# Optimization experiments

Hardware: AMD Instinct MI355X
Metric: run time of the kernel (lower is better)

## Reference

```python
import jax, jax.numpy as jnp
import numpy as np
from jax import lax

B, T, I, H, C = 64, 512, 512, 1024, 1000


def _lstm_layer(x, W_ih, W_hh, b_ih, b_hh):
    # x: [B, T, in]; W_ih: [4H, in]; W_hh: [4H, H]; biases: [4H]
    # Precompute input projections for all timesteps (one big GEMM).
    xW = jnp.einsum('bti,gi->btg', x, W_ih) + b_ih + b_hh  # [B, T, 4H]
    h0 = jnp.zeros((x.shape[0], W_hh.shape[1]), x.dtype)
    c0 = jnp.zeros_like(h0)

    def step(carry, xw_t):
        h, c = carry
        gates = xw_t + h @ W_hh.T  # [B, 4H]
        i, f, g, o = jnp.split(gates, 4, axis=-1)  # PyTorch gate order i,f,g,o
        i = jax.nn.sigmoid(i)
        f = jax.nn.sigmoid(f)
        g = jnp.tanh(g)
        o = jax.nn.sigmoid(o)
        c = f * c + i * g
        h = o * jnp.tanh(c)
        return (h, c), h

    (h_T, c_T), hs = lax.scan(step, (h0, c0), jnp.swapaxes(xW, 0, 1))
    return jnp.swapaxes(hs, 0, 1), h_T  # [B, T, H], [B, H]


def setup_inputs() -> dict:
    key = jax.random.key(0)
    ks = jax.random.split(key, 11)
    s_i = 1.0 / np.sqrt(H)
    u = lambda k, shape: jax.random.uniform(k, shape, jnp.float32, -s_i, s_i)
    return {
        'x': jax.random.normal(ks[0], (B, T, I), jnp.float32),
        'W_ih0': u(ks[1], (4 * H, I)),
        'W_hh0': u(ks[2], (4 * H, H)),
        'b_ih0': u(ks[3], (4 * H,)),
        'b_hh0': u(ks[4], (4 * H,)),
        'W_ih1': u(ks[5], (4 * H, H)),
        'W_hh1': u(ks[6], (4 * H, H)),
        'b_ih1': u(ks[7], (4 * H,)),
        'b_hh1': u(ks[8], (4 * H,)),
        'W_d': u(ks[9], (C, H)),
        'b_d': u(ks[10], (C,)),
    }


def reference(x, W_ih0, W_hh0, b_ih0, b_hh0, W_ih1, W_hh1, b_ih1, b_hh1, W_d, b_d):
    h1_seq, _ = _lstm_layer(x, W_ih0, W_hh0, b_ih0, b_hh0)
    _, h_last = _lstm_layer(h1_seq, W_ih1, W_hh1, b_ih1, b_hh1)
    return h_last @ W_d.T + b_d  # [B, num_classes]
```

## Files before the change

### kernel.cpp

```cpp
#include <hip/hip_runtime.h>

typedef short short8 __attribute__((ext_vector_type(8)));
typedef float f32x4 __attribute__((ext_vector_type(4)));
typedef float f32x16 __attribute__((ext_vector_type(16)));
typedef int i32x4 __attribute__((ext_vector_type(4)));
typedef unsigned short u16;

#define NBLK 256
#define BDIM 512
#define BB 64
#define TT 512
#define II 512
#define HH 1024
#define NCLS 1000
#define HBUF (BB*HH)

__device__ __forceinline__ u16 f2bf(float f) {
  union { float f; unsigned u; } v; v.f = f;
  unsigned u = v.u;
  u += 0x7fffu + ((u >> 16) & 1u);
  return (u16)(u >> 16);
}

__device__ __forceinline__ short8 cvt8(f32x4 a, f32x4 b) {
  short8 v;
  v[0] = (short)f2bf(a[0]); v[1] = (short)f2bf(a[1]);
  v[2] = (short)f2bf(a[2]); v[3] = (short)f2bf(a[3]);
  v[4] = (short)f2bf(b[0]); v[5] = (short)f2bf(b[1]);
  v[6] = (short)f2bf(b[2]); v[7] = (short)f2bf(b[3]);
  return v;
}

__device__ __forceinline__ unsigned ld_rlx(const unsigned* p) {
  return __hip_atomic_load(p, __ATOMIC_RELAXED, __HIP_MEMORY_SCOPE_AGENT);
}
__device__ __forceinline__ void st_rlx(unsigned* p, unsigned v) {
  __hip_atomic_store(p, v, __ATOMIC_RELAXED, __HIP_MEMORY_SCOPE_AGENT);
}
__device__ __forceinline__ void wave_wait_ge(const unsigned* p, unsigned tgt) {
  while (ld_rlx(p) < tgt) __builtin_amdgcn_s_sleep(1);
}

__global__ void cvt_x(const float* __restrict__ x, u16* __restrict__ xb, int n8) {
  int i = blockIdx.x * blockDim.x + threadIdx.x;
  const int stride = gridDim.x * blockDim.x;
  for (; i < n8; i += stride) {
    f32x4 a = ((const f32x4*)x)[2 * i];
    f32x4 b = ((const f32x4*)x)[2 * i + 1];
    ((short8*)xb)[i] = cvt8(a, b);
  }
}

#define ISSUE8(arr, OFF)                                                     \
  _Pragma("unroll") for (int i_ = 0; i_ < 8; ++i_)                           \
    asm volatile("global_load_dwordx4 %0, %1, off sc0 sc1"                   \
                 : "=v"(arr[i_]) : "v"(lanep + ((OFF) + i_) * 16));
#define MFMA8(arr, OFF)                                                      \
  _Pragma("unroll") for (int i_ = 0; i_ < 8; ++i_) {                         \
    union { i32x4 q; short8 s; } u_; u_.q = arr[i_];                         \
    acc = __builtin_amdgcn_mfma_f32_32x32x16_bf16(u_.s, breg[B0 + (OFF) + i_],\
                                                  acc, 0, 0, 0); }
#define VMWAIT0 asm volatile("s_waitcnt vmcnt(0)" ::: "memory")
#define VMWAIT8 asm volatile("s_waitcnt vmcnt(8)" ::: "memory")
#define SCHEDB  __builtin_amdgcn_sched_barrier(0)

template<int N, int B0, int MH>
__device__ __forceinline__ void run_coh(const u16* lanep,
                                        const short8 (&breg)[MH], f32x16& acc) {
  static_assert(N == 8 || N == 16 || N == 24 || N == 32, "");
  i32x4 avA[8], avB[8];
  if constexpr (N == 8) {
    ISSUE8(avA, 0);
    VMWAIT0; SCHEDB; MFMA8(avA, 0);
  } else if constexpr (N == 16) {
    ISSUE8(avA, 0); ISSUE8(avB, 8);
    VMWAIT8; SCHEDB; MFMA8(avA, 0);
    VMWAIT0; SCHEDB; MFMA8(avB, 8);
  } else if constexpr (N == 24) {
    ISSUE8(avA, 0); ISSUE8(avB, 8);
    VMWAIT8; SCHEDB; MFMA8(avA, 0); ISSUE8(avA, 16);
    VMWAIT8; SCHEDB; MFMA8(avB, 8);
    VMWAIT0; SCHEDB; MFMA8(avA, 16);
  } else {
    ISSUE8(avA, 0); ISSUE8(avB, 8);
    VMWAIT8; SCHEDB; MFMA8(avA, 0); ISSUE8(avA, 16);
    VMWAIT8; SCHEDB; MFMA8(avB, 8); ISSUE8(avB, 24);
    VMWAIT8; SCHEDB; MFMA8(avA, 16);
    VMWAIT0; SCHEDB; MFMA8(avB, 24);
  }
}

template<int N, int B0, int MH>
__device__ __forceinline__ void run_pb(const u16* lanep,
                                       const short8 (&breg)[MH], f32x16& acc) {
#pragma unroll
  for (int i = 0; i < N; ++i) {
    short8 av = *(const short8*)(lanep + i * 16);
    acc = __builtin_amdgcn_mfma_f32_32x32x16_bf16(av, breg[B0 + i], acc, 0, 0, 0);
  }
}

template<int N, int B0, int MH>
__device__ __forceinline__ void run_pf(const float* lanep,
                                       const short8 (&breg)[MH], f32x16& acc) {
#pragma unroll
  for (int i = 0; i < N; ++i) {
    short8 av = cvt8(*(const f32x4*)(lanep + i * 16),
                     *(const f32x4*)(lanep + i * 16 + 4));
    acc = __builtin_amdgcn_mfma_f32_32x32x16_bf16(av, breg[B0 + i], acc, 0, 0, 0);
  }
}

template<bool XBF>
__global__ __launch_bounds__(BDIM, 2) void lstm2_fused(
    const float* __restrict__ x, const u16* __restrict__ xb,
    const float* __restrict__ Wih0, const float* __restrict__ Whh0,
    const float* __restrict__ bih0, const float* __restrict__ bhh0,
    const float* __restrict__ Wih1, const float* __restrict__ Whh1,
    const float* __restrict__ bih1, const float* __restrict__ bhh1,
    u16* __restrict__ ring,
    u16* __restrict__ h1buf,
    float* __restrict__ h1f,
    unsigned* __restrict__ bar)
{
  __shared__ float g4[4][32][68];
  __shared__ float blds[64];

  const bool isL1 = (blockIdx.x >= 128);
  const int wgl = isL1 ? (int)blockIdx.x - 128 : (int)blockIdx.x;
  const int ug = wgl >> 1, bg = wgl & 1;
  const int j0 = ug * 16;
  const int rowoff = bg * 32;

  const int lane = threadIdx.x & 63;
  const int wid = threadIdx.x >> 6;
  const int gr = wid & 1, kq = wid >> 1;
  const int sub8 = (lane >> 5) << 3;
  const int rl = gr * 32 + (lane & 31);
  const int rglob = ((rl >> 4) << 10) + j0 + (rl & 15);
  const int arow = rowoff + (lane & 31);

  if (threadIdx.x < 64) {
    int u = threadIdx.x;
    int r = ((u >> 4) << 10) + j0 + (u & 15);
    blds[u] = isL1 ? (bih1[r] + bhh1[r]) : (bih0[r] + bhh0[r]);
  }
  __syncthreads();

  const int tb = threadIdx.x >> 4;
  const int tu = threadIdx.x & 15;

  unsigned* const arrA = bar;
  unsigned* const relA = bar + 64;
  unsigned* const arrB = bar + 128;
  unsigned* const relB = bar + 192;

  float c_state = 0.f;

  auto step_tail = [&](const f32x16& acc, u16* hout, unsigned ringtgt, bool wf,
                       unsigned* arr, unsigned* rel, int t) {
    const int col = lane & 31;
    const int rbase = (lane >> 5) << 2;
#pragma unroll
    for (int r = 0; r < 16; ++r) {
      int brow = rbase + (r & 3) + ((r >> 2) << 3);
      g4[kq][brow][gr * 32 + col] = acc[r];
    }
    __syncthreads();
    float gv[4];
#pragma unroll
    for (int g = 0; g < 4; ++g)
      gv[g] = g4[0][tb][g * 16 + tu] + g4[1][tb][g * 16 + tu]
            + g4[2][tb][g * 16 + tu] + g4[3][tb][g * 16 + tu]
            + blds[g * 16 + tu];
    float gi = 1.f / (1.f + __expf(-gv[0]));
    float gf = 1.f / (1.f + __expf(-gv[1]));
    float e2 = __expf(2.f * fminf(15.f, fmaxf(-15.f, gv[2])));
    float gg = (e2 - 1.f) / (e2 + 1.f);
    float go = 1.f / (1.f + __expf(-gv[3]));
    c_state = gf * c_state + gi * gg;
    float e2c = __expf(2.f * fminf(15.f, fmaxf(-15.f, c_state)));
    float th = (e2c - 1.f) / (e2c + 1.f);
    float hval = go * th;
    if (ringtgt) wave_wait_ge(relB, ringtgt);
    unsigned hu = (unsigned)f2bf(hval);
    unsigned nbv = (unsigned)__shfl_xor((int)hu, 1);
    if ((tu & 1) == 0) {
      unsigned packed = hu | (nbv << 16);
      unsigned* dst = (unsigned*)(hout + (size_t)(rowoff + tb) * HH + j0 + tu);
      st_rlx(dst, packed);
    }
    if (wf) h1f[(size_t)(rowoff + tb) * HH + j0 + tu] = hval;
    __syncthreads();
    if (threadIdx.x == 0) {
      unsigned old = atomicAdd(arr, 1u);
      if (old == (unsigned)(128 * (t + 1) - 1)) st_rlx(rel, (unsigned)(t + 1));
    }
  };

  if (!isL1) {
    short8 breg[24];
#pragma unroll
    for (int i = 0; i < 24; ++i) {
      int k = kq * 384 + i * 16 + sub8;
      const float* src = (k < II) ? (Wih0 + (size_t)rglob * II + k)
                                  : (Whh0 + (size_t)rglob * HH + (k - II));
      breg[i] = cvt8(*(const f32x4*)src, *(const f32x4*)(src + 4));
    }

    for (int t = 0; t < TT; ++t) {
      f32x16 acc = {};
      const u16* hb = ring + (size_t)((t + 2) % 3) * HBUF + (size_t)arow * HH;
      if (XBF) {
        const u16* xl = xb + (size_t)arow * ((size_t)TT * II) + (size_t)t * II
                        + kq * 384 + sub8;
        if (kq == 0)      run_pb<24, 0>(xl, breg, acc);
        else if (kq == 1) { run_pb<8, 0>(xl, breg, acc);
                            wave_wait_ge(relA, (unsigned)t);
                            run_coh<16, 8>(hb + 0 + sub8, breg, acc); }
        else if (kq == 2) { wave_wait_ge(relA, (unsigned)t);
                            run_coh<24, 0>(hb + 256 + sub8, breg, acc); }
        else              { wave_wait_ge(relA, (unsigned)t);
                            run_coh<24, 0>(hb + 640 + sub8, breg, acc); }
      } else {
        const float* xl = x + (size_t)arow * ((size_t)TT * II) + (size_t)t * II
                          + kq * 384 + sub8;
        if (kq == 0)      run_pf<24, 0>(xl, breg, acc);
        else if (kq == 1) { run_pf<8, 0>(xl, breg, acc);
                            wave_wait_ge(relA, (unsigned)t);
                            run_coh<16, 8>(hb + 0 + sub8, breg, acc); }
        else if (kq == 2) { wave_wait_ge(relA, (unsigned)t);
                            run_coh<24, 0>(hb + 256 + sub8, breg, acc); }
        else              { wave_wait_ge(relA, (unsigned)t);
                            run_coh<24, 0>(hb + 640 + sub8, breg, acc); }
      }
      step_tail(acc, ring + (size_t)(t % 3) * HBUF,
                (t >= 3) ? (unsigned)(t - 2) : 0u, false, arrA, relA, t);
    }
  } else {
    short8 breg[32];
#pragma unroll
    for (int i = 0; i < 32; ++i) {
      int k = kq * 512 + i * 16 + sub8;
      const float* src = (k < HH) ? (Wih1 + (size_t)rglob * HH + k)
                                  : (Whh1 + (size_t)rglob * HH + (k - HH));
      breg[i] = cvt8(*(const f32x4*)src, *(const f32x4*)(src + 4));
    }

    for (int t = 0; t < TT; ++t) {
      f32x16 acc = {};
      if (kq < 2) {
        wave_wait_ge(relA, (unsigned)(t + 1));
        const u16* lp = ring + (size_t)(t % 3) * HBUF + (size_t)arow * HH
                        + kq * 512 + sub8;
        run_coh<32, 0>(lp, breg, acc);
      } else {
        wave_wait_ge(relB, (unsigned)t);
        const u16* lp = h1buf + (size_t)((t + 1) & 1) * HBUF
                        + (size_t)arow * HH + (kq - 2) * 512 + sub8;
        run_coh<32, 0>(lp, breg, acc);
      }
      step_tail(acc, h1buf + (size_t)(t & 1) * HBUF, 0u, t == TT - 1,
                arrB, relB, t);
    }
  }
}

__global__ void dense_out(const float* __restrict__ h1, const float* __restrict__ Wd,
                          const float* __restrict__ bd, float* __restrict__ out)
{
  const int b  = threadIdx.x & 63;
  const int cl = threadIdx.x >> 6;
  const int cc = blockIdx.x * 4 + cl;
  float acc = 0.f;
  const float* hrow = h1 + (size_t)b * HH;
  const float* wrow = Wd + (size_t)cc * HH;
#pragma unroll 8
  for (int k = 0; k < HH; k += 4) {
    f32x4 hv = *(const f32x4*)(hrow + k);
    f32x4 wv = *(const f32x4*)(wrow + k);
    acc += hv[0] * wv[0] + hv[1] * wv[1] + hv[2] * wv[2] + hv[3] * wv[3];
  }
  out[(size_t)b * NCLS + cc] = acc + bd[cc];
}

extern "C" void kernel_launch(void* const* d_in, const int* in_sizes, int n_in,
                              void* d_out, int out_size, void* d_ws, size_t ws_size,
                              hipStream_t stream)
{
  (void)in_sizes; (void)n_in; (void)out_size;
  const float* x    = (const float*)d_in[0];
  const float* Wih0 = (const float*)d_in[1];
  const float* Whh0 = (const float*)d_in[2];
  const float* bih0 = (const float*)d_in[3];
  const float* bhh0 = (const float*)d_in[4];
  const float* Wih1 = (const float*)d_in[5];
  const float* Whh1 = (const float*)d_in[6];
  const float* bih1 = (const float*)d_in[7];
  const float* bhh1 = (const float*)d_in[8];
  const float* Wd   = (const float*)d_in[9];
  const float* bd   = (const float*)d_in[10];

  unsigned* bar = (unsigned*)d_ws;
  float* h1f  = (float*)((char*)d_ws + 4096);
  u16* h1buf  = (u16*)((char*)d_ws + 272 * 1024);
  u16* ring   = (u16*)((char*)d_ws + 528 * 1024);
  u16* xb     = (u16*)((char*)d_ws + (1u << 20));

  const size_t needA = (1u << 20) + (size_t)BB * TT * II * 2;
  const bool tierA = (ws_size >= needA);

  hipMemsetAsync(d_ws, 0, 912 * 1024, stream);

  if (tierA) {
    hipLaunchKernelGGL(cvt_x, dim3(2048), dim3(256), 0, stream,
                       x, xb, (int)((size_t)BB * TT * II / 8));
    hipLaunchKernelGGL((lstm2_fused<true>), dim3(NBLK), dim3(BDIM), 0, stream,
                       x, xb, Wih0, Whh0, bih0, bhh0, Wih1, Whh1, bih1, bhh1,
                       ring, h1buf, h1f, bar);
  } else {
    hipLaunchKernelGGL((lstm2_fused<false>), dim3(NBLK), dim3(BDIM), 0, stream,
                       x, xb, Wih0, Whh0, bih0, bhh0, Wih1, Whh1, bih1, bhh1,
                       ring, h1buf, h1f, bar);
  }
  hipLaunchKernelGGL(dense_out, dim3(250), dim3(256), 0, stream, h1f, Wd, bd,
                     (float*)d_out);
}
```

Measured before the change: 4.669 ms.

## Split K evenly across waves so each handles both input and recurrent parts

Changes how the K dimension is split across the four waves in both LSTM layers. Each wave now processes an equal slice of the input projection and an equal slice of the recurrent term, instead of some waves doing only input work while others wait and do only recurrent work. This lets every wave do its independent input work before waiting on the previous step's hidden state, which shortens the post-wait critical path of the recurrence. In exchange, all waves now block on the synchronisation flag, and the layer-1 waves wait on two flags in sequence.

```diff
diff --git a/kernel.cpp b/kernel.cpp
--- a/kernel.cpp
+++ b/kernel.cpp
@@ -201,38 +201,34 @@
   if (!isL1) {
     short8 breg[24];
 #pragma unroll
-    for (int i = 0; i < 24; ++i) {
-      int k = kq * 384 + i * 16 + sub8;
-      const float* src = (k < II) ? (Wih0 + (size_t)rglob * II + k)
-                                  : (Whh0 + (size_t)rglob * HH + (k - II));
-      breg[i] = cvt8(*(const f32x4*)src, *(const f32x4*)(src + 4));
+    for (int i = 0; i < 8; ++i) {
+      int k = kq * 128 + i * 16 + sub8;
+      breg[i] = cvt8(*(const f32x4*)(Wih0 + (size_t)rglob * II + k),
+                     *(const f32x4*)(Wih0 + (size_t)rglob * II + k + 4));
+    }
+#pragma unroll
+    for (int i = 0; i < 16; ++i) {
+      int k = kq * 256 + i * 16 + sub8;
+      breg[8 + i] = cvt8(*(const f32x4*)(Whh0 + (size_t)rglob * HH + k),
+                         *(const f32x4*)(Whh0 + (size_t)rglob * HH + k + 4));
     }
 
     for (int t = 0; t < TT; ++t) {
       f32x16 acc = {};
-      const u16* hb = ring + (size_t)((t + 2) % 3) * HBUF + (size_t)arow * HH;
       if (XBF) {
         const u16* xl = xb + (size_t)arow * ((size_t)TT * II) + (size_t)t * II
-                        + kq * 384 + sub8;
-        if (kq == 0)      run_pb<24, 0>(xl, breg, acc);
-        else if (kq == 1) { run_pb<8, 0>(xl, breg, acc);
-                            wave_wait_ge(relA, (unsigned)t);
-                            run_coh<16, 8>(hb + 0 + sub8, breg, acc); }
-        else if (kq == 2) { wave_wait_ge(relA, (unsigned)t);
-                            run_coh<24, 0>(hb + 256 + sub8, breg, acc); }
-        else              { wave_wait_ge(relA, (unsigned)t);
-                            run_coh<24, 0>(hb + 640 + sub8, breg, acc); }
+                        + kq * 128 + sub8;
+        run_pb<8, 0>(xl, breg, acc);
       } else {
         const float* xl = x + (size_t)arow * ((size_t)TT * II) + (size_t)t * II
-                          + kq * 384 + sub8;
-        if (kq == 0)      run_pf<24, 0>(xl, breg, acc);
-        else if (kq == 1) { run_pf<8, 0>(xl, breg, acc);
-                            wave_wait_ge(relA, (unsigned)t);
-                            run_coh<16, 8>(hb + 0 + sub8, breg, acc); }
-        else if (kq == 2) { wave_wait_ge(relA, (unsigned)t);
-                            run_coh<24, 0>(hb + 256 + sub8, breg, acc); }
-        else              { wave_wait_ge(relA, (unsigned)t);
-                            run_coh<24, 0>(hb + 640 + sub8, breg, acc); }
+                          + kq * 128 + sub8;
+        run_pf<8, 0>(xl, breg, acc);
+      }
+      wave_wait_ge(relA, (unsigned)t);
+      {
+        const u16* hb = ring + (size_t)((t + 2) % 3) * HBUF + (size_t)arow * HH
+                        + kq * 256 + sub8;
+        run_coh<16, 8>(hb, breg, acc);
       }
       step_tail(acc, ring + (size_t)(t % 3) * HBUF,
                 (t >= 3) ? (unsigned)(t - 2) : 0u, false, arrA, relA, t);
@@ -240,25 +236,31 @@
   } else {
     short8 breg[32];
 #pragma unroll
-    for (int i = 0; i < 32; ++i) {
-      int k = kq * 512 + i * 16 + sub8;
-      const float* src = (k < HH) ? (Wih1 + (size_t)rglob * HH + k)
-                                  : (Whh1 + (size_t)rglob * HH + (k - HH));
-      breg[i] = cvt8(*(const f32x4*)src, *(const f32x4*)(src + 4));
+    for (int i = 0; i < 16; ++i) {
+      int k = kq * 256 + i * 16 + sub8;
+      breg[i] = cvt8(*(const f32x4*)(Wih1 + (size_t)rglob * HH + k),
+                     *(const f32x4*)(Wih1 + (size_t)rglob * HH + k + 4));
+    }
+#pragma unroll
+    for (int i = 0; i < 16; ++i) {
+      int k = kq * 256 + i * 16 + sub8;
+      breg[16 + i] = cvt8(*(const f32x4*)(Whh1 + (size_t)rglob * HH + k),
+                          *(const f32x4*)(Whh1 + (size_t)rglob * HH + k + 4));
     }
 
     for (int t = 0; t < TT; ++t) {
       f32x16 acc = {};
-      if (kq < 2) {
-        wave_wait_ge(relA, (unsigned)(t + 1));
+      wave_wait_ge(relA, (unsigned)(t + 1));
+      {
         const u16* lp = ring + (size_t)(t % 3) * HBUF + (size_t)arow * HH
-                        + kq * 512 + sub8;
-        run_coh<32, 0>(lp, breg, acc);
-      } else {
-        wave_wait_ge(relB, (unsigned)t);
+                        + kq * 256 + sub8;
+        run_coh<16, 0>(lp, breg, acc);
+      }
+      wave_wait_ge(relB, (unsigned)t);
+      {
         const u16* lp = h1buf + (size_t)((t + 1) & 1) * HBUF
-                        + (size_t)arow * HH + (kq - 2) * 512 + sub8;
-        run_coh<32, 0>(lp, breg, acc);
+                        + (size_t)arow * HH + kq * 256 + sub8;
+        run_coh<16, 16>(lp, breg, acc);
       }
       step_tail(acc, h1buf + (size_t)(t & 1) * HBUF, 0u, t == TT - 1,
                 arrB, relB, t);
```

Measured after the change: 4.909 ms. 5.1% more time.
